# Kernel tuning notes

Hardware: AMD Instinct MI355X
Metric: run time of the kernel (lower is better)

## Reference

```python
import jax, jax.numpy as jnp
import numpy as np

DIM = 512

def setup_inputs() -> dict:
    key = jax.random.key(0)
    ks = jax.random.split(key, 7)
    s = 1.0 / np.sqrt(DIM)
    x1 = jax.random.normal(ks[0], (2, 8192, DIM), dtype=jnp.float32)
    Wk = jax.random.uniform(ks[1], (DIM, DIM), jnp.float32, -s, s)
    bk = jax.random.uniform(ks[2], (DIM,), jnp.float32, -s, s)
    Wq = jax.random.uniform(ks[3], (DIM, DIM), jnp.float32, -s, s)
    bq = jax.random.uniform(ks[4], (DIM,), jnp.float32, -s, s)
    Wv = jax.random.uniform(ks[5], (DIM, DIM), jnp.float32, -s, s)
    bv = jax.random.uniform(ks[6], (DIM,), jnp.float32, -s, s)
    return {"x1": x1, "Wk": Wk, "bk": bk, "Wq": Wq, "bq": bq, "Wv": Wv, "bv": bv}

def reference(x1, Wk, bk, Wq, bq, Wv, bv):
    # Linear layers: y = x @ W^T + b (torch convention)
    k = jnp.einsum('bsd,ed->bse', x1, Wk) + bk
    q = jnp.einsum('bsd,ed->bse', x1, Wq) + bq
    v = jnp.einsum('bsd,ed->bse', x1, Wv) + bv
    # Faithful to source: qk = k @ q^T (k as rows, q as columns)
    qk = jnp.einsum('bsd,btd->bst', k, q)  # [B, S, S]
    attn = jax.nn.softmax(qk, axis=-1)
    # dropout(p=0.1) treated as identity (eval mode) for determinism
    out = jnp.einsum('bst,btd->bsd', attn, v)
    mask = jnp.zeros((4, 4), dtype=jnp.float32)
    return (out, mask)
```

## Files before the change

### kernel.cpp

```cpp
#include <hip/hip_runtime.h>
#include <hip/hip_bf16.h>

typedef _Float16 f16x8 __attribute__((ext_vector_type(8)));
typedef _Float16 f16x4 __attribute__((ext_vector_type(4)));
typedef float f32x4 __attribute__((ext_vector_type(4)));
typedef float f32x16 __attribute__((ext_vector_type(16)));

#define MFMA16(A, B, C) __builtin_amdgcn_mfma_f32_16x16x32_f16((A), (B), (C), 0, 0, 0)
#define MFMA32(A, B, C) __builtin_amdgcn_mfma_f32_32x32x16_f16((A), (B), (C), 0, 0, 0)

#define DIMD 512
#define SEQ  8192
#define MTOT 16384

#define GLOAD16(gp, lp) __builtin_amdgcn_global_load_lds( \
    (const __attribute__((address_space(1))) void*)(gp),  \
    (__attribute__((address_space(3))) void*)(lp), 16, 0, 0)

#define LGKM0_BAR() do { \
    asm volatile("s_waitcnt lgkmcnt(0)" ::: "memory"); \
    __builtin_amdgcn_s_barrier(); \
    asm volatile("" ::: "memory"); } while (0)

__global__ __launch_bounds__(256) void proj_kernel(
    const float* __restrict__ x1,
    const float* __restrict__ Wk, const float* __restrict__ bk,
    const float* __restrict__ Wq, const float* __restrict__ bq,
    const float* __restrict__ Wv, const float* __restrict__ bv,
    _Float16* __restrict__ Kh, _Float16* __restrict__ Qh, _Float16* __restrict__ Vt)
{
    const int g = blockIdx.z;
    const float* W    = (g == 0) ? Wk : (g == 1) ? Wq : Wv;
    const float* bias = (g == 0) ? bk : (g == 1) ? bq : bv;

    const int m0 = blockIdx.x * 128;
    const int n0 = blockIdx.y * 128;
    const int t  = threadIdx.x;
    const int lane = t & 63;
    const int w  = t >> 6;
    const int wr = w >> 1, wc = w & 1;
    const int lr = lane & 15;
    const int lkg = lane >> 4;
    const int lk = lkg * 8;

    __shared__ _Float16 Ah[128][40];
    __shared__ _Float16 Bh[128][40];

    f32x4 acc[4][4] = {};

    const int sr  = t >> 1;
    const int skh = (t & 1) * 16;

    for (int k0 = 0; k0 < DIMD; k0 += 32) {
        const float* sa = x1 + (size_t)(m0 + sr) * DIMD + k0 + skh;
        const float* sb = W  + (size_t)(n0 + sr) * DIMD + k0 + skh;
        _Float16 ta[16], tb[16];
        #pragma unroll
        for (int i = 0; i < 4; i++) {
            f32x4 va = *(const f32x4*)(sa + i * 4);
            f32x4 vb = *(const f32x4*)(sb + i * 4);
            #pragma unroll
            for (int u = 0; u < 4; u++) {
                ta[i * 4 + u] = (_Float16)va[u];
                tb[i * 4 + u] = (_Float16)vb[u];
            }
        }
        __syncthreads();
        *(f16x8*)&Ah[sr][skh]     = *(f16x8*)&ta[0];
        *(f16x8*)&Ah[sr][skh + 8] = *(f16x8*)&ta[8];
        *(f16x8*)&Bh[sr][skh]     = *(f16x8*)&tb[0];
        *(f16x8*)&Bh[sr][skh + 8] = *(f16x8*)&tb[8];
        __syncthreads();

        f16x8 af[4], bf[4];
        #pragma unroll
        for (int i = 0; i < 4; i++) af[i] = *(const f16x8*)&Ah[wr * 64 + i * 16 + lr][lk];
        #pragma unroll
        for (int j = 0; j < 4; j++) bf[j] = *(const f16x8*)&Bh[wc * 64 + j * 16 + lr][lk];
        #pragma unroll
        for (int i = 0; i < 4; i++)
            #pragma unroll
            for (int j = 0; j < 4; j++)
                acc[i][j] = MFMA16(af[i], bf[j], acc[i][j]);
    }

    const int col0 = n0 + wc * 64;
    const int row0 = m0 + wr * 64;
    #pragma unroll
    for (int j = 0; j < 4; j++) {
        float bval = bias[col0 + j * 16 + lr];
        #pragma unroll
        for (int i = 0; i < 4; i++) {
            #pragma unroll
            for (int jj = 0; jj < 4; jj++) {
                int mrow = row0 + i * 16 + lkg * 4 + jj;
                int e    = col0 + j * 16 + lr;
                float val = acc[i][j][jj] + bval;
                if (g == 2) {
                    Vt[(size_t)(mrow >> 13) * DIMD * SEQ + (size_t)e * SEQ + (mrow & 8191)] =
                        (_Float16)val;
                } else {
                    _Float16* outp = (g == 0) ? Kh : Qh;
                    outp[(size_t)mrow * DIMD + e] = (_Float16)val;
                }
            }
        }
    }
}

template<int SPLIT>
__global__ __launch_bounds__(512, 2) void flash_kernel(
    const _Float16* __restrict__ Kh,
    const _Float16* __restrict__ Qh,
    const _Float16* __restrict__ Vt,
    float* __restrict__ out,
    _Float16* __restrict__ Opart,
    float* __restrict__ Ml)
{
    const int B   = blockIdx.x;
    const int xcd = B & 7;
    constexpr int XPC = (SPLIT == 2) ? 2 : 4;
    const int combo = xcd / XPC;
    const int batch = (SPLIT == 2) ? (combo >> 1) : combo;
    const int half  = (SPLIT == 2) ? (combo & 1) : 0;
    const int qbl   = (B >> 3) * XPC + (xcd % XPC);
    const int R0    = batch * SEQ + qbl * 128;

    const int t    = threadIdx.x;
    const int lane = t & 63;
    const int w    = t >> 6;
    const int q31  = lane & 31;
    const int h    = lane >> 5;
    const int mg   = w >> 1;
    const int kh   = w & 1;

    __shared__ _Float16 Klds[64][512];
    __shared__ _Float16 Vlds[512][64];
    __shared__ _Float16 Plds[128][64];
    __shared__ float Mbuf[8][32];
    __shared__ float Sbuf[8][32];
    __shared__ float Scl[128];
    __shared__ int NeedR;

    const _Float16* Qb = Qh + (size_t)batch * SEQ * DIMD;
    const _Float16* Vb = Vt + (size_t)batch * DIMD * SEQ;

    const int qrow = R0 + mg * 32 + q31;
    f16x8 qf[32];
    #pragma unroll
    for (int ks = 0; ks < 32; ks++)
        qf[ks] = *(const f16x8*)(Kh + (size_t)qrow * DIMD + ks * 16 + h * 8);

    f32x16 Oacc[4][2] = {};
    float m_ = -1e30f, l_ = 0.f;

    const int t0base = half * (SEQ / SPLIT);
    const int NT = (SEQ / SPLIT) / 64;

    #define STAGE_K(it)                                                        \
    {                                                                          \
        const int t0s = t0base + (it) * 64;                                    \
        _Pragma("unroll")                                                      \
        for (int i = 0; i < 8; i++) {                                          \
            const int r = w * 8 + i;                                           \
            const char* src = (const char*)(Qb + (size_t)(t0s + r) * DIMD)     \
                              + ((lane ^ (r & 15)) << 4);                      \
            GLOAD16(src, (char*)&Klds[r][0]);                                  \
        }                                                                      \
    }
    #define STAGE_V(it)                                                        \
    {                                                                          \
        const int t0v = t0base + (it) * 64;                                    \
        _Pragma("unroll")                                                      \
        for (int i = 0; i < 8; i++) {                                          \
            const int D0 = (w * 8 + i) * 8;                                    \
            const int dr = D0 + (lane >> 3);                                   \
            const _Float16* src = Vb + (size_t)dr * SEQ + t0v                  \
                                  + 8 * ((lane & 7) ^ (dr & 7));               \
            GLOAD16(src, (char*)&Vlds[D0][0]);                                 \
        }                                                                      \
    }

    STAGE_K(0);
    STAGE_V(0);
    if (t == 0) NeedR = 0;

    for (int it = 0; it < NT; ++it) {
        const int itn = (it + 1 < NT) ? it + 1 : 0;

        asm volatile("s_waitcnt vmcnt(0)" ::: "memory");
        __builtin_amdgcn_s_barrier();
        asm volatile("" ::: "memory");

        f32x16 sT = {};
        const int krow = kh * 32 + q31;
        #pragma unroll
        for (int ks = 0; ks < 32; ks++) {
            const int ch = ((2 * ks + h) ^ (lane & 15)) << 4;
            f16x8 af = *(const f16x8*)((const char*)&Klds[krow][0] + ch);
            sT = MFMA32(af, qf[ks], sT);
        }

        float mx = sT[0];
        #pragma unroll
        for (int r = 1; r < 16; r++) mx = fmaxf(mx, sT[r]);
        mx = fmaxf(mx, __shfl_xor(mx, 32, 64));
        if (lane < 32) Mbuf[w][lane] = mx;

        LGKM0_BAR();

        STAGE_K(itn);

        float pm = fmaxf(mx, Mbuf[w ^ 1][q31]);
        float scale = 1.f;
        if (pm > m_ + 8.f) { scale = __expf(m_ - pm); m_ = pm; }
        float ps = 0.f;
        f16x4 pq[4];
        #pragma unroll
        for (int r = 0; r < 16; r++) {
            float p = __expf(sT[r] - m_);
            ps += p;
            pq[r >> 2][r & 3] = (_Float16)p;
        }
        ps += __shfl_xor(ps, 32, 64);
        if (lane < 32) {
            Sbuf[w][lane] = ps;
            if (kh == 0) Scl[mg * 32 + lane] = scale;
        }
        if (__any(scale != 1.f) && lane == 0) NeedR = 1;
        #pragma unroll
        for (int rq = 0; rq < 4; rq++) {
            int s  = kh * 8 + 2 * rq + h;
            int sp = s ^ (lane & 15);
            *(f16x4*)((char*)&Plds[mg * 32 + q31][0] + sp * 8) = pq[rq];
        }

        LGKM0_BAR();

        l_ = l_ * scale + (ps + Sbuf[w ^ 1][q31]);
        if (NeedR) {
            #pragma unroll
            for (int m2 = 0; m2 < 4; m2++) {
                #pragma unroll
                for (int rq = 0; rq < 4; rq++) {
                    f32x4 s4 = *(const f32x4*)&Scl[m2 * 32 + rq * 8 + 4 * h];
                    #pragma unroll
                    for (int n = 0; n < 2; n++)
                        #pragma unroll
                        for (int e = 0; e < 4; e++)
                            Oacc[m2][n][rq * 4 + e] *= s4[e];
                }
            }
        }

        #pragma unroll
        for (int ks = 0; ks < 4; ks++) {
            f16x8 vb[2];
            #pragma unroll
            for (int n = 0; n < 2; n++) {
                const int dd = w * 64 + n * 32 + q31;
                const int ch = ((2 * ks + h) ^ (dd & 7)) << 4;
                vb[n] = *(const f16x8*)((const char*)&Vlds[dd][0] + ch);
            }
            #pragma unroll
            for (int m2 = 0; m2 < 4; m2++) {
                const char* prow = (const char*)&Plds[m2 * 32 + q31][0];
                const int s0 = ((4 * ks + 2 * h)     ^ (lane & 15)) * 8;
                const int s1 = ((4 * ks + 2 * h + 1) ^ (lane & 15)) * 8;
                f16x4 a0 = *(const f16x4*)(prow + s0);
                f16x4 a1 = *(const f16x4*)(prow + s1);
                f16x8 pa;
                #pragma unroll
                for (int e = 0; e < 4; e++) { pa[e] = a0[e]; pa[e + 4] = a1[e]; }
                #pragma unroll
                for (int n = 0; n < 2; n++)
                    Oacc[m2][n] = MFMA32(pa, vb[n], Oacc[m2][n]);
            }
        }

        LGKM0_BAR();
        if (t == 0) NeedR = 0;
        STAGE_V(itn);
    }

    if (kh == 0 && lane < 32) {
        Scl[mg * 32 + lane] = 1.f / l_;
        if (SPLIT > 1) {
            int R = R0 + mg * 32 + lane;
            Ml[((size_t)half * MTOT + R) * 2]     = m_;
            Ml[((size_t)half * MTOT + R) * 2 + 1] = l_;
        }
    }
    LGKM0_BAR();

    #pragma unroll
    for (int m2 = 0; m2 < 4; m2++) {
        #pragma unroll
        for (int rq = 0; rq < 4; rq++) {
            f32x4 li = *(const f32x4*)&Scl[m2 * 32 + rq * 8 + 4 * h];
            #pragma unroll
            for (int e = 0; e < 4; e++) {
                int row = R0 + m2 * 32 + rq * 8 + 4 * h + e;
                #pragma unroll
                for (int n = 0; n < 2; n++) {
                    int d = w * 64 + n * 32 + q31;
                    float val = Oacc[m2][n][rq * 4 + e] * li[e];
                    if (SPLIT == 1) {
                        out[(size_t)row * DIMD + d] = val;
                    } else {
                        Opart[((size_t)half * MTOT + row) * DIMD + d] = (_Float16)val;
                    }
                }
            }
        }
    }
    #undef STAGE_K
    #undef STAGE_V
}

__global__ __launch_bounds__(256) void combine_kernel(
    const _Float16* __restrict__ Opart, const float* __restrict__ Ml,
    float* __restrict__ out)
{
    size_t idx = (size_t)blockIdx.x * 256 + threadIdx.x;
    size_t e0 = idx * 8;
    int R = (int)(e0 >> 9);
    float m0 = Ml[(size_t)R * 2],            l0 = Ml[(size_t)R * 2 + 1];
    float m1 = Ml[((size_t)MTOT + R) * 2],   l1 = Ml[((size_t)MTOT + R) * 2 + 1];
    float M  = fmaxf(m0, m1);
    float a0 = __expf(m0 - M) * l0;
    float a1 = __expf(m1 - M) * l1;
    float inv = 1.f / (a0 + a1);
    a0 *= inv; a1 *= inv;
    f16x8 o0 = *(const f16x8*)(Opart + e0);
    f16x8 o1 = *(const f16x8*)(Opart + (size_t)MTOT * DIMD + e0);
    f32x4 r0, r1;
    #pragma unroll
    for (int u = 0; u < 4; u++) r0[u] = a0 * (float)o0[u] + a1 * (float)o1[u];
    #pragma unroll
    for (int u = 0; u < 4; u++) r1[u] = a0 * (float)o0[u + 4] + a1 * (float)o1[u + 4];
    *(f32x4*)(out + e0) = r0;
    *(f32x4*)(out + e0 + 4) = r1;
}

extern "C" void kernel_launch(void* const* d_in, const int* in_sizes, int n_in,
                              void* d_out, int out_size, void* d_ws, size_t ws_size,
                              hipStream_t stream) {
    (void)in_sizes; (void)n_in; (void)out_size;
    const float* x1 = (const float*)d_in[0];
    const float* Wk = (const float*)d_in[1];
    const float* bk = (const float*)d_in[2];
    const float* Wq = (const float*)d_in[3];
    const float* bq = (const float*)d_in[4];
    const float* Wv = (const float*)d_in[5];
    const float* bv = (const float*)d_in[6];
    float* out = (float*)d_out;

    _Float16* Kh = (_Float16*)d_ws;
    _Float16* Qh = Kh + (size_t)MTOT * DIMD;
    _Float16* Vt = Qh + (size_t)MTOT * DIMD;

    const size_t base = (size_t)MTOT * DIMD * 2 * 3;
    const size_t opart_bytes = (size_t)2 * MTOT * DIMD * sizeof(_Float16);
    const size_t need2 = base + opart_bytes + (size_t)2 * MTOT * 2 * sizeof(float);
    _Float16* Opart = (_Float16*)((char*)d_ws + base);
    float*    Ml    = (float*)((char*)d_ws + base + opart_bytes);
    const int split2 = (ws_size >= need2);

    hipMemsetAsync((char*)d_out + (size_t)MTOT * DIMD * sizeof(float), 0, 64, stream);

    dim3 pg(128, 4, 3);
    proj_kernel<<<pg, 256, 0, stream>>>(x1, Wk, bk, Wq, bq, Wv, bv, Kh, Qh, Vt);

    if (split2) {
        flash_kernel<2><<<dim3(256), 512, 0, stream>>>(Kh, Qh, Vt, out, Opart, Ml);
        combine_kernel<<<4096, 256, 0, stream>>>(Opart, Ml, out);
    } else {
        flash_kernel<1><<<dim3(128), 512, 0, stream>>>(Kh, Qh, Vt, out, Opart, Ml);
    }
}
```

Before: 1.023 ms.

## Add four-way key-split flash attention with generalized combine kernel

Adds a SPLIT=4 mode in which each query block's key range is divided into four parts, giving 512 workgroups instead of 256. The aim is better occupancy on a GPU with many compute units, where 256 blocks at two per CU underfill the device. The combine kernel is templated to merge S partial outputs using their max and sum statistics. The cost is more fp16 partial-output traffic, a heavier combine pass, and a larger workspace; the code falls back to the two-way split if the workspace is too small.

```diff
diff --git a/kernel.cpp b/kernel.cpp
--- a/kernel.cpp
+++ b/kernel.cpp
@@ -119,12 +119,22 @@
 {
     const int B   = blockIdx.x;
     const int xcd = B & 7;
-    constexpr int XPC = (SPLIT == 2) ? 2 : 4;
-    const int combo = xcd / XPC;
-    const int batch = (SPLIT == 2) ? (combo >> 1) : combo;
-    const int half  = (SPLIT == 2) ? (combo & 1) : 0;
-    const int qbl   = (B >> 3) * XPC + (xcd % XPC);
-    const int R0    = batch * SEQ + qbl * 128;
+    int batch, s_idx, qbl;
+    if constexpr (SPLIT == 4) {
+        batch = xcd >> 2;
+        s_idx = xcd & 3;
+        qbl   = B >> 3;
+    } else if constexpr (SPLIT == 2) {
+        const int combo = xcd >> 1;
+        batch = combo >> 1;
+        s_idx = combo & 1;
+        qbl   = (B >> 3) * 2 + (xcd & 1);
+    } else {
+        batch = xcd >> 2;
+        s_idx = 0;
+        qbl   = (B >> 3) * 4 + (xcd & 3);
+    }
+    const int R0 = batch * SEQ + qbl * 128;
 
     const int t    = threadIdx.x;
     const int lane = t & 63;
@@ -154,7 +164,7 @@
     f32x16 Oacc[4][2] = {};
     float m_ = -1e30f, l_ = 0.f;
 
-    const int t0base = half * (SEQ / SPLIT);
+    const int t0base = s_idx * (SEQ / SPLIT);
     const int NT = (SEQ / SPLIT) / 64;
 
     #define STAGE_K(it)                                                        \
@@ -287,8 +297,8 @@
         Scl[mg * 32 + lane] = 1.f / l_;
         if (SPLIT > 1) {
             int R = R0 + mg * 32 + lane;
-            Ml[((size_t)half * MTOT + R) * 2]     = m_;
-            Ml[((size_t)half * MTOT + R) * 2 + 1] = l_;
+            Ml[((size_t)s_idx * MTOT + R) * 2]     = m_;
+            Ml[((size_t)s_idx * MTOT + R) * 2 + 1] = l_;
         }
     }
     LGKM0_BAR();
@@ -308,7 +318,7 @@
                     if (SPLIT == 1) {
                         out[(size_t)row * DIMD + d] = val;
                     } else {
-                        Opart[((size_t)half * MTOT + row) * DIMD + d] = (_Float16)val;
+                        Opart[((size_t)s_idx * MTOT + row) * DIMD + d] = (_Float16)val;
                     }
                 }
             }
@@ -318,6 +328,7 @@
     #undef STAGE_V
 }
 
+template<int S>
 __global__ __launch_bounds__(256) void combine_kernel(
     const _Float16* __restrict__ Opart, const float* __restrict__ Ml,
     float* __restrict__ out)
@@ -325,20 +336,29 @@
     size_t idx = (size_t)blockIdx.x * 256 + threadIdx.x;
     size_t e0 = idx * 8;
     int R = (int)(e0 >> 9);
-    float m0 = Ml[(size_t)R * 2],            l0 = Ml[(size_t)R * 2 + 1];
-    float m1 = Ml[((size_t)MTOT + R) * 2],   l1 = Ml[((size_t)MTOT + R) * 2 + 1];
-    float M  = fmaxf(m0, m1);
-    float a0 = __expf(m0 - M) * l0;
-    float a1 = __expf(m1 - M) * l1;
-    float inv = 1.f / (a0 + a1);
-    a0 *= inv; a1 *= inv;
-    f16x8 o0 = *(const f16x8*)(Opart + e0);
-    f16x8 o1 = *(const f16x8*)(Opart + (size_t)MTOT * DIMD + e0);
+    float m[S], l[S];
+    float M = -1e30f;
+    #pragma unroll
+    for (int hh = 0; hh < S; hh++) {
+        m[hh] = Ml[((size_t)hh * MTOT + R) * 2];
+        l[hh] = Ml[((size_t)hh * MTOT + R) * 2 + 1];
+        M = fmaxf(M, m[hh]);
+    }
+    float a[S], Z = 0.f;
+    #pragma unroll
+    for (int hh = 0; hh < S; hh++) { a[hh] = __expf(m[hh] - M) * l[hh]; Z += a[hh]; }
+    float inv = 1.f / Z;
+    float acc[8] = {};
+    #pragma unroll
+    for (int hh = 0; hh < S; hh++) {
+        f16x8 o = *(const f16x8*)(Opart + (size_t)hh * MTOT * DIMD + e0);
+        float ah = a[hh] * inv;
+        #pragma unroll
+        for (int u = 0; u < 8; u++) acc[u] += ah * (float)o[u];
+    }
     f32x4 r0, r1;
     #pragma unroll
-    for (int u = 0; u < 4; u++) r0[u] = a0 * (float)o0[u] + a1 * (float)o1[u];
-    #pragma unroll
-    for (int u = 0; u < 4; u++) r1[u] = a0 * (float)o0[u + 4] + a1 * (float)o1[u + 4];
+    for (int u = 0; u < 4; u++) { r0[u] = acc[u]; r1[u] = acc[u + 4]; }
     *(f32x4*)(out + e0) = r0;
     *(f32x4*)(out + e0 + 4) = r1;
 }
@@ -361,21 +381,26 @@
     _Float16* Vt = Qh + (size_t)MTOT * DIMD;
 
     const size_t base = (size_t)MTOT * DIMD * 2 * 3;
-    const size_t opart_bytes = (size_t)2 * MTOT * DIMD * sizeof(_Float16);
-    const size_t need2 = base + opart_bytes + (size_t)2 * MTOT * 2 * sizeof(float);
+    const size_t opart_slice = (size_t)MTOT * DIMD * sizeof(_Float16);
     _Float16* Opart = (_Float16*)((char*)d_ws + base);
-    float*    Ml    = (float*)((char*)d_ws + base + opart_bytes);
-    const int split2 = (ws_size >= need2);
 
     hipMemsetAsync((char*)d_out + (size_t)MTOT * DIMD * sizeof(float), 0, 64, stream);
 
     dim3 pg(128, 4, 3);
     proj_kernel<<<pg, 256, 0, stream>>>(x1, Wk, bk, Wq, bq, Wv, bv, Kh, Qh, Vt);
 
-    if (split2) {
+    const size_t need4 = base + 4 * (opart_slice + (size_t)MTOT * 8);
+    const size_t need2 = base + 2 * (opart_slice + (size_t)MTOT * 8);
+    if (ws_size >= need4) {
+        float* Ml = (float*)((char*)d_ws + base + 4 * opart_slice);
+        flash_kernel<4><<<dim3(512), 512, 0, stream>>>(Kh, Qh, Vt, out, Opart, Ml);
+        combine_kernel<4><<<4096, 256, 0, stream>>>(Opart, Ml, out);
+    } else if (ws_size >= need2) {
+        float* Ml = (float*)((char*)d_ws + base + 2 * opart_slice);
         flash_kernel<2><<<dim3(256), 512, 0, stream>>>(Kh, Qh, Vt, out, Opart, Ml);
-        combine_kernel<<<4096, 256, 0, stream>>>(Opart, Ml, out);
+        combine_kernel<2><<<4096, 256, 0, stream>>>(Opart, Ml, out);
     } else {
+        float* Ml = (float*)((char*)d_ws + base);
         flash_kernel<1><<<dim3(128), 512, 0, stream>>>(Kh, Qh, Vt, out, Opart, Ml);
     }
 }
```

Result: slower. 1.063 ms (+3.9%).

## Pack Q and V^T per 64-row tile into contiguous blocks for flash staging

Applied to the files above, without the earlier changes.

The projection kernel now writes Q and transposed V into a tile-packed buffer: each 64-key tile holds its 64x512 Q rows followed by its 512x64 V^T block in one contiguous 128KB region. Flash staging then reads one contiguous region per tile instead of strided rows across the whole sequence, aiming for better DRAM locality and fewer page and TLB misses. It also drops the wasted prefetch after the last iteration and marks the K loads, partial-output stores and combine loads as nontemporal. The projection V writes stay scattered, and the pack layout ties both kernels to a fixed 64-row tile size.

```diff
diff --git a/kernel.cpp b/kernel.cpp
--- a/kernel.cpp
+++ b/kernel.cpp
@@ -12,6 +12,7 @@
 #define DIMD 512
 #define SEQ  8192
 #define MTOT 16384
+#define TILE_F16 65536
 
 #define GLOAD16(gp, lp) __builtin_amdgcn_global_load_lds( \
     (const __attribute__((address_space(1))) void*)(gp),  \
@@ -27,7 +28,7 @@
     const float* __restrict__ Wk, const float* __restrict__ bk,
     const float* __restrict__ Wq, const float* __restrict__ bq,
     const float* __restrict__ Wv, const float* __restrict__ bv,
-    _Float16* __restrict__ Kh, _Float16* __restrict__ Qh, _Float16* __restrict__ Vt)
+    _Float16* __restrict__ Kh, _Float16* __restrict__ pack)
 {
     const int g = blockIdx.z;
     const float* W    = (g == 0) ? Wk : (g == 1) ? Wq : Wv;
@@ -96,12 +97,17 @@
                 int mrow = row0 + i * 16 + lkg * 4 + jj;
                 int e    = col0 + j * 16 + lr;
                 float val = acc[i][j][jj] + bval;
-                if (g == 2) {
-                    Vt[(size_t)(mrow >> 13) * DIMD * SEQ + (size_t)e * SEQ + (mrow & 8191)] =
-                        (_Float16)val;
+                _Float16 hv = (_Float16)val;
+                const int batch = mrow >> 13;
+                const int s     = mrow & 8191;
+                if (g == 0) {
+                    Kh[(size_t)mrow * DIMD + e] = hv;
+                } else if (g == 1) {
+                    pack[((size_t)(batch * 128 + (s >> 6))) * TILE_F16
+                         + (size_t)(s & 63) * DIMD + e] = hv;
                 } else {
-                    _Float16* outp = (g == 0) ? Kh : Qh;
-                    outp[(size_t)mrow * DIMD + e] = (_Float16)val;
+                    pack[((size_t)(batch * 128 + (s >> 6))) * TILE_F16
+                         + 32768 + (size_t)e * 64 + (s & 63)] = hv;
                 }
             }
         }
@@ -111,20 +117,25 @@
 template<int SPLIT>
 __global__ __launch_bounds__(512, 2) void flash_kernel(
     const _Float16* __restrict__ Kh,
-    const _Float16* __restrict__ Qh,
-    const _Float16* __restrict__ Vt,
+    const _Float16* __restrict__ pack,
     float* __restrict__ out,
     _Float16* __restrict__ Opart,
     float* __restrict__ Ml)
 {
     const int B   = blockIdx.x;
     const int xcd = B & 7;
-    constexpr int XPC = (SPLIT == 2) ? 2 : 4;
-    const int combo = xcd / XPC;
-    const int batch = (SPLIT == 2) ? (combo >> 1) : combo;
-    const int half  = (SPLIT == 2) ? (combo & 1) : 0;
-    const int qbl   = (B >> 3) * XPC + (xcd % XPC);
-    const int R0    = batch * SEQ + qbl * 128;
+    int batch, s_idx, qbl;
+    if constexpr (SPLIT == 2) {
+        const int combo = xcd >> 1;
+        batch = combo >> 1;
+        s_idx = combo & 1;
+        qbl   = (B >> 3) * 2 + (xcd & 1);
+    } else {
+        batch = xcd >> 2;
+        s_idx = 0;
+        qbl   = (B >> 3) * 4 + (xcd & 3);
+    }
+    const int R0 = batch * SEQ + qbl * 128;
 
     const int t    = threadIdx.x;
     const int lane = t & 63;
@@ -142,42 +153,41 @@
     __shared__ float Scl[128];
     __shared__ int NeedR;
 
-    const _Float16* Qb = Qh + (size_t)batch * SEQ * DIMD;
-    const _Float16* Vb = Vt + (size_t)batch * DIMD * SEQ;
-
     const int qrow = R0 + mg * 32 + q31;
     f16x8 qf[32];
     #pragma unroll
     for (int ks = 0; ks < 32; ks++)
-        qf[ks] = *(const f16x8*)(Kh + (size_t)qrow * DIMD + ks * 16 + h * 8);
+        qf[ks] = __builtin_nontemporal_load(
+            (const f16x8*)(Kh + (size_t)qrow * DIMD + ks * 16 + h * 8));
 
     f32x16 Oacc[4][2] = {};
     float m_ = -1e30f, l_ = 0.f;
 
-    const int t0base = half * (SEQ / SPLIT);
+    const int t0base = s_idx * (SEQ / SPLIT);
     const int NT = (SEQ / SPLIT) / 64;
+    const size_t packbase = (size_t)batch * 128;
 
     #define STAGE_K(it)                                                        \
     {                                                                          \
-        const int t0s = t0base + (it) * 64;                                    \
+        const char* tb = (const char*)(pack +                                  \
+            (packbase + (size_t)((t0base >> 6) + (it))) * TILE_F16);           \
         _Pragma("unroll")                                                      \
         for (int i = 0; i < 8; i++) {                                          \
             const int r = w * 8 + i;                                           \
-            const char* src = (const char*)(Qb + (size_t)(t0s + r) * DIMD)     \
-                              + ((lane ^ (r & 15)) << 4);                      \
-            GLOAD16(src, (char*)&Klds[r][0]);                                  \
+            GLOAD16(tb + r * 1024 + ((lane ^ (r & 15)) << 4),                  \
+                    (char*)&Klds[r][0]);                                       \
         }                                                                      \
     }
     #define STAGE_V(it)                                                        \
     {                                                                          \
-        const int t0v = t0base + (it) * 64;                                    \
+        const char* tb = (const char*)(pack +                                  \
+            (packbase + (size_t)((t0base >> 6) + (it))) * TILE_F16) + 65536;   \
         _Pragma("unroll")                                                      \
         for (int i = 0; i < 8; i++) {                                          \
             const int D0 = (w * 8 + i) * 8;                                    \
             const int dr = D0 + (lane >> 3);                                   \
-            const _Float16* src = Vb + (size_t)dr * SEQ + t0v                  \
-                                  + 8 * ((lane & 7) ^ (dr & 7));               \
-            GLOAD16(src, (char*)&Vlds[D0][0]);                                 \
+            GLOAD16(tb + dr * 128 + (((lane & 7) ^ (dr & 7)) << 4),            \
+                    (char*)&Vlds[D0][0]);                                      \
         }                                                                      \
     }
 
@@ -186,8 +196,6 @@
     if (t == 0) NeedR = 0;
 
     for (int it = 0; it < NT; ++it) {
-        const int itn = (it + 1 < NT) ? it + 1 : 0;
-
         asm volatile("s_waitcnt vmcnt(0)" ::: "memory");
         __builtin_amdgcn_s_barrier();
         asm volatile("" ::: "memory");
@@ -209,7 +217,7 @@
 
         LGKM0_BAR();
 
-        STAGE_K(itn);
+        if (it + 1 < NT) STAGE_K(it + 1);
 
         float pm = fmaxf(mx, Mbuf[w ^ 1][q31]);
         float scale = 1.f;
@@ -280,15 +288,15 @@
 
         LGKM0_BAR();
         if (t == 0) NeedR = 0;
-        STAGE_V(itn);
+        if (it + 1 < NT) STAGE_V(it + 1);
     }
 
     if (kh == 0 && lane < 32) {
         Scl[mg * 32 + lane] = 1.f / l_;
         if (SPLIT > 1) {
             int R = R0 + mg * 32 + lane;
-            Ml[((size_t)half * MTOT + R) * 2]     = m_;
-            Ml[((size_t)half * MTOT + R) * 2 + 1] = l_;
+            __builtin_nontemporal_store(m_, &Ml[((size_t)s_idx * MTOT + R) * 2]);
+            __builtin_nontemporal_store(l_, &Ml[((size_t)s_idx * MTOT + R) * 2 + 1]);
         }
     }
     LGKM0_BAR();
@@ -308,7 +316,9 @@
                     if (SPLIT == 1) {
                         out[(size_t)row * DIMD + d] = val;
                     } else {
-                        Opart[((size_t)half * MTOT + row) * DIMD + d] = (_Float16)val;
+                        __builtin_nontemporal_store(
+                            (_Float16)val,
+                            &Opart[((size_t)s_idx * MTOT + row) * DIMD + d]);
                     }
                 }
             }
@@ -332,8 +342,9 @@
     float a1 = __expf(m1 - M) * l1;
     float inv = 1.f / (a0 + a1);
     a0 *= inv; a1 *= inv;
-    f16x8 o0 = *(const f16x8*)(Opart + e0);
-    f16x8 o1 = *(const f16x8*)(Opart + (size_t)MTOT * DIMD + e0);
+    f16x8 o0 = __builtin_nontemporal_load((const f16x8*)(Opart + e0));
+    f16x8 o1 = __builtin_nontemporal_load(
+        (const f16x8*)(Opart + (size_t)MTOT * DIMD + e0));
     f32x4 r0, r1;
     #pragma unroll
     for (int u = 0; u < 4; u++) r0[u] = a0 * (float)o0[u] + a1 * (float)o1[u];
@@ -356,26 +367,26 @@
     const float* bv = (const float*)d_in[6];
     float* out = (float*)d_out;
 
-    _Float16* Kh = (_Float16*)d_ws;
-    _Float16* Qh = Kh + (size_t)MTOT * DIMD;
-    _Float16* Vt = Qh + (size_t)MTOT * DIMD;
+    _Float16* Kh   = (_Float16*)d_ws;
+    _Float16* pack = Kh + (size_t)MTOT * DIMD;
 
     const size_t base = (size_t)MTOT * DIMD * 2 * 3;
-    const size_t opart_bytes = (size_t)2 * MTOT * DIMD * sizeof(_Float16);
-    const size_t need2 = base + opart_bytes + (size_t)2 * MTOT * 2 * sizeof(float);
+    const size_t opart_slice = (size_t)MTOT * DIMD * sizeof(_Float16);
     _Float16* Opart = (_Float16*)((char*)d_ws + base);
-    float*    Ml    = (float*)((char*)d_ws + base + opart_bytes);
-    const int split2 = (ws_size >= need2);
 
     hipMemsetAsync((char*)d_out + (size_t)MTOT * DIMD * sizeof(float), 0, 64, stream);
 
     dim3 pg(128, 4, 3);
-    proj_kernel<<<pg, 256, 0, stream>>>(x1, Wk, bk, Wq, bq, Wv, bv, Kh, Qh, Vt);
-
-    if (split2) {
-        flash_kernel<2><<<dim3(256), 512, 0, stream>>>(Kh, Qh, Vt, out, Opart, Ml);
+    proj_kernel<<<pg, 256, 0, stream>>>(x1, Wk, bk, Wq, bq, Wv, bv, Kh, pack);
+
+    const size_t ml_bytes = (size_t)2 * MTOT * 2 * sizeof(float);
+    const size_t need2 = base + 2 * opart_slice + ml_bytes;
+    if (ws_size >= need2) {
+        float* Ml = (float*)((char*)d_ws + base + 2 * opart_slice);
+        flash_kernel<2><<<dim3(256), 512, 0, stream>>>(Kh, pack, out, Opart, Ml);
         combine_kernel<<<4096, 256, 0, stream>>>(Opart, Ml, out);
     } else {
-        flash_kernel<1><<<dim3(128), 512, 0, stream>>>(Kh, Qh, Vt, out, Opart, Ml);
+        float* Ml = (float*)((char*)d_ws + base);
+        flash_kernel<1><<<dim3(128), 512, 0, stream>>>(Kh, pack, out, Opart, Ml);
     }
 }
```

New measurement: 949.5 us. 7.2% less time.
